# Kernel tuning notes

Measured on AMD Instinct MI355X. Metric: run time of the kernel, lower is better.

The kernel has to match this reference:

```python
import jax, jax.numpy as jnp
import numpy as np

B, P, C = 32, 8, 2048
D, H, W = 9, 11, 9
L = D * H * W  # 891
HID = C * P // 2  # 8192


def setup_inputs() -> dict:
    key = jax.random.key(0)
    k_x, k1w, k1b, k2w, k2b = jax.random.split(key, 5)
    x = jax.random.normal(k_x, (B, C, D, H, W), dtype=jnp.float32)
    fc1_w = jax.random.normal(k1w, (HID, C), dtype=jnp.float32) * 0.02
    fc1_b = jax.random.normal(k1b, (HID,), dtype=jnp.float32) * 0.02
    fc2_w = jax.random.normal(k2w, (C * P, HID), dtype=jnp.float32) * 0.02
    fc2_b = jax.random.normal(k2b, (C * P,), dtype=jnp.float32) * 0.02
    return {"x": x, "fc1_w": fc1_w, "fc1_b": fc1_b, "fc2_w": fc2_w, "fc2_b": fc2_b}


def reference(x, fc1_w, fc1_b, fc2_w, fc2_b):
    b = x.shape[0]
    # global average pool over the 9x11x9 volume -> (B, C)
    pooled = x.reshape(b, C, L).mean(axis=-1)
    h = jax.nn.sigmoid(pooled @ fc1_w.T + fc1_b)
    g = jax.nn.sigmoid(h @ fc2_w.T + fc2_b)          # (B, P*C)
    grouping_result = g.reshape(b, P, C)               # unfold(-1, C, C)
    # fused weighted channel reduction: avoids (B, P, C, 891) intermediate.
    # original: (grouping * conv_matrix) then AdaptiveAvgPool3d((891,1,1))
    # == mean over channels of grouping[b,p,c] * x[b,c,l]
    flat = x.reshape(b, C, L)
    weighted = jnp.einsum('bpc,bcl->bpl', grouping_result, flat) / C
    weighted = weighted.reshape(b, P, D, H, W)
    return (grouping_result, weighted)
```

## Files before the change

### kernel.cpp

```cpp
#include <hip/hip_runtime.h>
#include <hip/hip_bf16.h>

#define BB 32
#define CC 2048
#define LL 891
#define PP 8
#define HIDN 8192
#define NOUT 16384

typedef __attribute__((ext_vector_type(4))) float f32x4;
typedef __attribute__((ext_vector_type(8))) __bf16 bf16x8;

__global__ __launch_bounds__(256) void pool_kernel(const float* __restrict__ x,
                                                   __hip_bfloat16* __restrict__ pooled) {
  int wid = threadIdx.x >> 6, lane = threadIdx.x & 63;
  int row = blockIdx.x * 4 + wid;
  const float* r = x + (long)row * LL;
  int align = (4 - ((row * 3) & 3)) & 3;
  int nvec = (LL - align) >> 2;
  int rem = LL - align - (nvec << 2);
  const float4* v = (const float4*)(r + align);
  float s = 0.f;
  for (int i = lane; i < nvec; i += 64) {
    float4 q = v[i];
    s += (q.x + q.y) + (q.z + q.w);
  }
  if (lane < align) s += r[lane];
  if (lane < rem) s += r[align + (nvec << 2) + lane];
#pragma unroll
  for (int off = 32; off > 0; off >>= 1) s += __shfl_xor(s, off);
  if (lane == 0) pooled[row] = __float2bfloat16(s * (1.0f / (float)LL));
}

__device__ __forceinline__ unsigned int bfbits(float f) {
  unsigned int x = __builtin_bit_cast(unsigned int, f);
  return (x + 0x7fffu + ((x >> 16) & 1u)) >> 16;
}

__global__ __launch_bounds__(256) void fc_kernel(const __hip_bfloat16* __restrict__ A,
                                                 const float* __restrict__ W,
                                                 float* __restrict__ partial,
                                                 int N, int K, int kc) {
  int lane = threadIdx.x & 63, wv = threadIdx.x >> 6;
  int n0 = blockIdx.x * 64 + wv * 16;
  int k0 = blockIdx.y * kc;
  int r = lane & 15, kg = lane >> 4;

  const float* Wp = W + (long)(n0 + r) * K + k0 + kg * 8;
  const __hip_bfloat16* Ap0 = A + (long)r * K + k0 + kg * 8;
  const __hip_bfloat16* Ap1 = Ap0 + 16 * (long)K;

  f32x4 acc0 = {0.f, 0.f, 0.f, 0.f};
  f32x4 acc1 = {0.f, 0.f, 0.f, 0.f};

#pragma unroll 2
  for (int ks = 0; ks < kc; ks += 32) {
    float4 w0 = *(const float4*)(Wp + ks);
    float4 w1 = *(const float4*)(Wp + ks + 4);
    int4 a0 = *(const int4*)(Ap0 + ks);
    int4 a1 = *(const int4*)(Ap1 + ks);
    int4 bw;
    bw.x = (int)(bfbits(w0.x) | (bfbits(w0.y) << 16));
    bw.y = (int)(bfbits(w0.z) | (bfbits(w0.w) << 16));
    bw.z = (int)(bfbits(w1.x) | (bfbits(w1.y) << 16));
    bw.w = (int)(bfbits(w1.z) | (bfbits(w1.w) << 16));
    bf16x8 bv = __builtin_bit_cast(bf16x8, bw);
    acc0 = __builtin_amdgcn_mfma_f32_16x16x32_bf16(__builtin_bit_cast(bf16x8, a0), bv, acc0, 0, 0, 0);
    acc1 = __builtin_amdgcn_mfma_f32_16x16x32_bf16(__builtin_bit_cast(bf16x8, a1), bv, acc1, 0, 0, 0);
  }

  long base = (long)blockIdx.y * 32 * N + n0 + r;
#pragma unroll
  for (int j = 0; j < 4; ++j) {
    int row = kg * 4 + j;
    partial[base + (long)row * N] = acc0[j];
    partial[base + (long)(row + 16) * N] = acc1[j];
  }
}

__global__ __launch_bounds__(256) void fc_reduce_kernel(const float* __restrict__ part,
                                                        int nsplit, int MN, int N,
                                                        const float* __restrict__ bias,
                                                        float* __restrict__ outF,
                                                        __hip_bfloat16* __restrict__ outB) {
  int idx = blockIdx.x * 256 + threadIdx.x;
  if (idx >= MN) return;
  float s = 0.f;
  for (int i = 0; i < nsplit; ++i) s += part[(long)i * MN + idx];
  s += bias[idx & (N - 1)];
  float v = 1.f / (1.f + __expf(-s));
  if (outF) outF[idx] = v;
  if (outB) outB[idx] = __float2bfloat16(v);
}

__global__ __launch_bounds__(256) void ein_partial_kernel(const float* __restrict__ x,
                                                          const float* __restrict__ g,
                                                          float* __restrict__ part) {
  int l = blockIdx.x * 256 + threadIdx.x;
  int b = blockIdx.y;
  int s = blockIdx.z;
  int c0 = s * 256;
  const float* xp = x + ((long)b * CC + c0) * LL + l;
  const float* gp = g + (long)b * NOUT + c0;
  bool act = l < LL;
  float acc[PP] = {0.f, 0.f, 0.f, 0.f, 0.f, 0.f, 0.f, 0.f};
#pragma unroll 4
  for (int i = 0; i < 256; ++i) {
    float xv = act ? xp[(long)i * LL] : 0.f;
#pragma unroll
    for (int p = 0; p < PP; ++p) acc[p] += gp[p * CC + i] * xv;
  }
  if (act) {
    float* pp = part + (long)(s * BB + b) * PP * LL + l;
#pragma unroll
    for (int p = 0; p < PP; ++p) pp[(long)p * LL] = acc[p];
  }
}

__global__ __launch_bounds__(256) void ein_reduce_kernel(const float* __restrict__ part,
                                                         float* __restrict__ outw) {
  int idx = blockIdx.x * 256 + threadIdx.x;
  float s = 0.f;
#pragma unroll
  for (int i = 0; i < 8; ++i) s += part[(long)i * (BB * PP * LL) + idx];
  outw[idx] = s * (1.0f / (float)CC);
}

extern "C" void kernel_launch(void* const* d_in, const int* in_sizes, int n_in,
                              void* d_out, int out_size, void* d_ws, size_t ws_size,
                              hipStream_t stream) {
  const float* x     = (const float*)d_in[0];
  const float* fc1_w = (const float*)d_in[1];
  const float* fc1_b = (const float*)d_in[2];
  const float* fc2_w = (const float*)d_in[3];
  const float* fc2_b = (const float*)d_in[4];
  float* out = (float*)d_out;

  char* ws = (char*)d_ws;
  __hip_bfloat16* pooled = (__hip_bfloat16*)ws;
  __hip_bfloat16* hbuf   = (__hip_bfloat16*)(ws + 131072);
  float* part            = (float*)(ws + 655360);

  pool_kernel<<<BB * CC / 4, 256, 0, stream>>>(x, pooled);

  fc_kernel<<<dim3(HIDN / 64, 8), 256, 0, stream>>>(pooled, fc1_w, part, HIDN, CC, CC / 8);
  fc_reduce_kernel<<<BB * HIDN / 256, 256, 0, stream>>>(part, 8, BB * HIDN, HIDN, fc1_b,
                                                        nullptr, hbuf);

  fc_kernel<<<dim3(NOUT / 64, 4), 256, 0, stream>>>(hbuf, fc2_w, part, NOUT, HIDN, HIDN / 4);
  fc_reduce_kernel<<<BB * NOUT / 256, 256, 0, stream>>>(part, 4, BB * NOUT, NOUT, fc2_b,
                                                        out, nullptr);

  ein_partial_kernel<<<dim3(4, BB, 8), 256, 0, stream>>>(x, out, part);
  ein_reduce_kernel<<<BB * PP * LL / 256, 256, 0, stream>>>(part, out + BB * PP * CC);
}
```

Before: 285.4 us.

## Stream FC weights with nontemporal loads, vectorize reductions, deepen split-K

FC weight tiles are now read with nontemporal loads and converted to bf16 with native casts instead of manual bit rounding. The FC loop unroll goes from 2 to 4. fc2 now splits K eight ways instead of four, so more blocks are in flight. The reduce kernels process four floats per thread with vector loads and stores, and the einsum partial loop unroll goes from 4 to 8. Together these target bandwidth on the 512MB fc2 weight stream and launch/instruction overhead, at the cost of more partial-sum traffic for fc2.

```diff
diff --git a/kernel.cpp b/kernel.cpp
--- a/kernel.cpp
+++ b/kernel.cpp
@@ -19,10 +19,10 @@
   int align = (4 - ((row * 3) & 3)) & 3;
   int nvec = (LL - align) >> 2;
   int rem = LL - align - (nvec << 2);
-  const float4* v = (const float4*)(r + align);
+  const f32x4* v = (const f32x4*)(r + align);
   float s = 0.f;
   for (int i = lane; i < nvec; i += 64) {
-    float4 q = v[i];
+    f32x4 q = v[i];
     s += (q.x + q.y) + (q.z + q.w);
   }
   if (lane < align) s += r[lane];
@@ -32,9 +32,15 @@
   if (lane == 0) pooled[row] = __float2bfloat16(s * (1.0f / (float)LL));
 }
 
-__device__ __forceinline__ unsigned int bfbits(float f) {
-  unsigned int x = __builtin_bit_cast(unsigned int, f);
-  return (x + 0x7fffu + ((x >> 16) & 1u)) >> 16;
+__device__ __forceinline__ f32x4 ldnt(const float* p) {
+  return __builtin_nontemporal_load((const f32x4*)p);
+}
+
+__device__ __forceinline__ bf16x8 cvt8(f32x4 a, f32x4 b) {
+  bf16x8 r;
+  r[0] = (__bf16)a.x; r[1] = (__bf16)a.y; r[2] = (__bf16)a.z; r[3] = (__bf16)a.w;
+  r[4] = (__bf16)b.x; r[5] = (__bf16)b.y; r[6] = (__bf16)b.z; r[7] = (__bf16)b.w;
+  return r;
 }
 
 __global__ __launch_bounds__(256) void fc_kernel(const __hip_bfloat16* __restrict__ A,
@@ -53,18 +59,13 @@
   f32x4 acc0 = {0.f, 0.f, 0.f, 0.f};
   f32x4 acc1 = {0.f, 0.f, 0.f, 0.f};
 
-#pragma unroll 2
+#pragma unroll 4
   for (int ks = 0; ks < kc; ks += 32) {
-    float4 w0 = *(const float4*)(Wp + ks);
-    float4 w1 = *(const float4*)(Wp + ks + 4);
+    f32x4 w0 = ldnt(Wp + ks);
+    f32x4 w1 = ldnt(Wp + ks + 4);
     int4 a0 = *(const int4*)(Ap0 + ks);
     int4 a1 = *(const int4*)(Ap1 + ks);
-    int4 bw;
-    bw.x = (int)(bfbits(w0.x) | (bfbits(w0.y) << 16));
-    bw.y = (int)(bfbits(w0.z) | (bfbits(w0.w) << 16));
-    bw.z = (int)(bfbits(w1.x) | (bfbits(w1.y) << 16));
-    bw.w = (int)(bfbits(w1.z) | (bfbits(w1.w) << 16));
-    bf16x8 bv = __builtin_bit_cast(bf16x8, bw);
+    bf16x8 bv = cvt8(w0, w1);
     acc0 = __builtin_amdgcn_mfma_f32_16x16x32_bf16(__builtin_bit_cast(bf16x8, a0), bv, acc0, 0, 0, 0);
     acc1 = __builtin_amdgcn_mfma_f32_16x16x32_bf16(__builtin_bit_cast(bf16x8, a1), bv, acc1, 0, 0, 0);
   }
@@ -83,14 +84,26 @@
                                                         const float* __restrict__ bias,
                                                         float* __restrict__ outF,
                                                         __hip_bfloat16* __restrict__ outB) {
-  int idx = blockIdx.x * 256 + threadIdx.x;
-  if (idx >= MN) return;
-  float s = 0.f;
-  for (int i = 0; i < nsplit; ++i) s += part[(long)i * MN + idx];
-  s += bias[idx & (N - 1)];
-  float v = 1.f / (1.f + __expf(-s));
-  if (outF) outF[idx] = v;
-  if (outB) outB[idx] = __float2bfloat16(v);
+  int i4 = blockIdx.x * 256 + threadIdx.x;
+  if (i4 * 4 >= MN) return;
+  f32x4 s = {0.f, 0.f, 0.f, 0.f};
+  for (int i = 0; i < nsplit; ++i) {
+    f32x4 v = *(const f32x4*)(part + (long)i * MN + i4 * 4);
+    s += v;
+  }
+  f32x4 bv = *(const f32x4*)(bias + ((i4 * 4) & (N - 1)));
+  f32x4 g;
+  g.x = 1.f / (1.f + __expf(-(s.x + bv.x)));
+  g.y = 1.f / (1.f + __expf(-(s.y + bv.y)));
+  g.z = 1.f / (1.f + __expf(-(s.z + bv.z)));
+  g.w = 1.f / (1.f + __expf(-(s.w + bv.w)));
+  if (outF) *(f32x4*)(outF + i4 * 4) = g;
+  if (outB) {
+    union { __hip_bfloat16 h[4]; unsigned long long u; } pk;
+    pk.h[0] = __float2bfloat16(g.x); pk.h[1] = __float2bfloat16(g.y);
+    pk.h[2] = __float2bfloat16(g.z); pk.h[3] = __float2bfloat16(g.w);
+    *((unsigned long long*)outB + i4) = pk.u;
+  }
 }
 
 __global__ __launch_bounds__(256) void ein_partial_kernel(const float* __restrict__ x,
@@ -104,7 +117,7 @@
   const float* gp = g + (long)b * NOUT + c0;
   bool act = l < LL;
   float acc[PP] = {0.f, 0.f, 0.f, 0.f, 0.f, 0.f, 0.f, 0.f};
-#pragma unroll 4
+#pragma unroll 8
   for (int i = 0; i < 256; ++i) {
     float xv = act ? xp[(long)i * LL] : 0.f;
 #pragma unroll
@@ -119,11 +132,17 @@
 
 __global__ __launch_bounds__(256) void ein_reduce_kernel(const float* __restrict__ part,
                                                          float* __restrict__ outw) {
-  int idx = blockIdx.x * 256 + threadIdx.x;
-  float s = 0.f;
+  int i4 = blockIdx.x * 256 + threadIdx.x;
+  if (i4 >= (BB * PP * LL) / 4) return;
+  f32x4 s = {0.f, 0.f, 0.f, 0.f};
 #pragma unroll
-  for (int i = 0; i < 8; ++i) s += part[(long)i * (BB * PP * LL) + idx];
-  outw[idx] = s * (1.0f / (float)CC);
+  for (int i = 0; i < 8; ++i) {
+    f32x4 v = *(const f32x4*)(part + (long)i * (BB * PP * LL) + i4 * 4);
+    s += v;
+  }
+  const float inv = 1.0f / (float)CC;
+  f32x4 o = s * inv;
+  *(f32x4*)(outw + i4 * 4) = o;
 }
 
 extern "C" void kernel_launch(void* const* d_in, const int* in_sizes, int n_in,
@@ -144,13 +163,13 @@
   pool_kernel<<<BB * CC / 4, 256, 0, stream>>>(x, pooled);
 
   fc_kernel<<<dim3(HIDN / 64, 8), 256, 0, stream>>>(pooled, fc1_w, part, HIDN, CC, CC / 8);
-  fc_reduce_kernel<<<BB * HIDN / 256, 256, 0, stream>>>(part, 8, BB * HIDN, HIDN, fc1_b,
-                                                        nullptr, hbuf);
+  fc_reduce_kernel<<<BB * HIDN / 1024, 256, 0, stream>>>(part, 8, BB * HIDN, HIDN, fc1_b,
+                                                         nullptr, hbuf);
 
-  fc_kernel<<<dim3(NOUT / 64, 4), 256, 0, stream>>>(hbuf, fc2_w, part, NOUT, HIDN, HIDN / 4);
-  fc_reduce_kernel<<<BB * NOUT / 256, 256, 0, stream>>>(part, 4, BB * NOUT, NOUT, fc2_b,
-                                                        out, nullptr);
+  fc_kernel<<<dim3(NOUT / 64, 8), 256, 0, stream>>>(hbuf, fc2_w, part, NOUT, HIDN, HIDN / 8);
+  fc_reduce_kernel<<<BB * NOUT / 1024, 256, 0, stream>>>(part, 8, BB * NOUT, NOUT, fc2_b,
+                                                         out, nullptr);
 
   ein_partial_kernel<<<dim3(4, BB, 8), 256, 0, stream>>>(x, out, part);
-  ein_reduce_kernel<<<BB * PP * LL / 256, 256, 0, stream>>>(part, out + BB * PP * CC);
+  ein_reduce_kernel<<<(BB * PP * LL / 4 + 255) / 256, 256, 0, stream>>>(part, out + BB * PP * CC);
 }
```

New measurement: 288.1 us. No clear change (+1.0%).
